# Performance work log

Measured on AMD Instinct MI355X. Metric: run time of the kernel, lower is better.

## Reference

```python
import jax, jax.numpy as jnp
import numpy as np

B, OP, MA, F_IN, F_OUT = 8, 400, 200, 64, 64


def setup_inputs() -> dict:
    key = jax.random.key(0)
    ks = jax.random.split(key, 8)
    x = jax.random.normal(ks[0], (B, OP, F_IN), dtype=jnp.float32)
    y = jax.random.normal(ks[1], (B, MA, F_IN), dtype=jnp.float32)
    z = jax.random.normal(ks[2], (B, OP, MA, F_IN), dtype=jnp.float32)
    op_ma_adj = jax.random.randint(ks[3], (B, OP, MA), 0, 2, dtype=jnp.int32)
    # xavier-uniform-ish params
    lim = float(np.sqrt(6.0 / (F_IN + F_OUT)))
    W_op = jax.random.uniform(ks[4], (F_IN, F_OUT), minval=-lim, maxval=lim, dtype=jnp.float32)
    W_ma = jax.random.uniform(ks[5], (F_IN, F_OUT), minval=-lim, maxval=lim, dtype=jnp.float32)
    W_edge = jax.random.uniform(ks[6], (F_IN, F_OUT), minval=-lim, maxval=lim, dtype=jnp.float32)
    lim_a = float(np.sqrt(6.0 / (1 + 3 * F_OUT)))
    att_vec = jax.random.uniform(ks[7], (3 * F_OUT,), minval=-lim_a, maxval=lim_a, dtype=jnp.float32)
    return {"x": x, "y": y, "z": z, "op_ma_adj": op_ma_adj,
            "W_op": W_op, "W_ma": W_ma, "W_edge": W_edge, "att_vec": att_vec}


def reference(x, y, z, op_ma_adj, W_op, W_ma, W_edge, att_vec):
    F = W_op.shape[1]
    h_op = jnp.einsum('bni,io->bno', x, W_op)                      # [B, op, F]
    h = jnp.einsum('bmi,io->bmo', y, W_ma)                         # [B, ma, F]
    h_edge = jnp.einsum('bnmi,io->bnmo', z, W_edge).transpose(0, 2, 1, 3)  # [B, ma, op, F]
    # attention score: concat([h_op, h_ma, h_edge]) @ a  ==  per-part dot products (no BxMAxOPx3F materialization)
    a_op, a_ma, a_edge = att_vec[:F], att_vec[F:2 * F], att_vec[2 * F:]
    e = (jnp.einsum('bnf,f->bn', h_op, a_op)[:, None, :]
         + jnp.einsum('bmf,f->bm', h, a_ma)[:, :, None]
         + jnp.einsum('bmnf,f->bmn', h_edge, a_edge))              # [B, ma, op]
    e = jax.nn.leaky_relu(e, negative_slope=0.01)
    adjT = op_ma_adj.transpose(0, 2, 1)                            # [B, ma, op]
    row_empty = jnp.all(adjT == 0, axis=-1, keepdims=True)         # [B, ma, 1]
    att = jnp.where(adjT > 0, e, -jnp.inf)
    att = jnp.where(row_empty, 0.0, att)                           # empty rows -> uniform softmax (matches torch)
    att = jax.nn.softmax(att, axis=-1)                             # [B, ma, op]
    h_op_edge = h_op[:, None, :, :] + h_edge                       # [B, ma, op, F]
    h_prime = jnp.einsum('bmn,bmnf->bmf', att, h_op_edge)          # [B, ma, F]
    h_prime = jnp.where(row_empty, 0.0, h_prime) + h
    return jax.nn.elu(h_prime)
```

## Files before the change

### kernel.cpp

```cpp
#include <hip/hip_runtime.h>
#include <math.h>

#define B_   8
#define OP_  400
#define MA_  200
#define ZROW (MA_ * 64)
#define NEGM -1.0e30f

__global__ __launch_bounds__(256) void precompute_k(
    const float* __restrict__ x, const float* __restrict__ y,
    const float* __restrict__ Wop, const float* __restrict__ Wma,
    const float* __restrict__ Wedge, const float* __restrict__ att,
    float* __restrict__ ws_we, float* __restrict__ ws_eop, float* __restrict__ ws_ema)
{
    __shared__ float w_s[192];
    const int tid = threadIdx.x, wv = tid >> 6, ln = tid & 63;
    if (tid < 192) {
        const int which = tid >> 6, i = tid & 63;
        const float* W = (which == 0) ? Wop : ((which == 1) ? Wma : Wedge);
        const float* a = att + which * 64;
        float acc = 0.f;
        #pragma unroll 8
        for (int f = 0; f < 64; ++f) acc = fmaf(W[i * 64 + f], a[f], acc);
        w_s[tid] = acc;
    }
    __syncthreads();
    if (blockIdx.x == 0 && tid < 64) ws_we[tid] = w_s[128 + tid];

    const int row = blockIdx.x * 4 + wv;
    if (row < B_ * OP_) {
        float s = x[(size_t)row * 64 + ln] * w_s[ln];
        #pragma unroll
        for (int o = 32; o > 0; o >>= 1) s += __shfl_xor(s, o, 64);
        if (ln == 0) ws_eop[row] = s;
    } else if (row < B_ * OP_ + B_ * MA_) {
        const int r2 = row - B_ * OP_;
        float s = y[(size_t)r2 * 64 + ln] * w_s[64 + ln];
        #pragma unroll
        for (int o = 32; o > 0; o >>= 1) s += __shfl_xor(s, o, 64);
        if (ln == 0) ws_ema[r2] = s;
    }
}

__global__ __launch_bounds__(256) void gat_fused(
    const float* __restrict__ x, const float* __restrict__ y,
    const float* __restrict__ z, const int* __restrict__ adj,
    const float* __restrict__ Wop, const float* __restrict__ Wma,
    const float* __restrict__ Wedge,
    const float* __restrict__ ws_we, const float* __restrict__ ws_eop,
    const float* __restrict__ ws_ema, float* __restrict__ out)
{
    __shared__ int   ln_s[4][104];
    __shared__ float le_s[4][104];
    __shared__ float mred[4], lred[4];
    __shared__ float vws[4][64], uws[4][64];
    __shared__ float vs_s[64], us_s[64], ys_s[64];
    __shared__ float pvt[4][64];

    const int tid = threadIdx.x, wv = tid >> 6, ln = tid & 63;
    const int bm = blockIdx.x;
    const int b = bm / MA_, m = bm % MA_;

    const float ema = ws_ema[bm];
    const float wl  = ws_we[ln];

    const int rbase = wv * 100;
    int cnt = 0;
    #pragma unroll
    for (int round = 0; round < 2; ++round) {
        const int lr = round * 64 + ln;
        const int n  = rbase + lr;
        bool a = false;
        if (lr < 100) a = (adj[((size_t)(b * OP_ + n)) * MA_ + m] != 0);
        const unsigned long long mask = __ballot(a);
        if (a) {
            const int pos = cnt + __popcll(mask & ((1ull << ln) - 1ull));
            ln_s[wv][pos] = n;
            le_s[wv][pos] = ws_eop[b * OP_ + n] + ema;
        }
        cnt += __popcll(mask);
    }
    const int cnt_p = (cnt + 3) & ~3;
    if (ln < cnt_p - cnt) {
        ln_s[wv][cnt + ln] = rbase;
        le_s[wv][cnt + ln] = NEGM;
    }

    const float* zb = z + ((size_t)b * OP_ * MA_ + m) * 64;
    const float* xb = x + (size_t)b * OP_ * 64;

    float M = NEGM, L = 0.f, v = 0.f, u = 0.f;

    #define UPD(zv, xv, eo) do {                                   \
        float s_ = (zv) * wl;                                      \
        s_ += __shfl_xor(s_, 1, 64);  s_ += __shfl_xor(s_, 2, 64); \
        s_ += __shfl_xor(s_, 4, 64);  s_ += __shfl_xor(s_, 8, 64); \
        s_ += __shfl_xor(s_, 16, 64); s_ += __shfl_xor(s_, 32, 64);\
        float e_ = s_ + (eo);                                      \
        e_ = (e_ >= 0.f) ? e_ : 0.01f * e_;                        \
        const float m2_ = fmaxf(M, e_);                            \
        const float c_  = __expf(M - m2_);                         \
        const float p_  = __expf(e_ - m2_);                        \
        L = fmaf(L, c_, p_);                                       \
        v = fmaf(v, c_, p_ * (zv));                                \
        u = fmaf(u, c_, p_ * (xv));                                \
        M = m2_;                                                   \
    } while (0)

    for (int i = 0; i < cnt_p; i += 4) {
        const int n0 = __builtin_amdgcn_readfirstlane(ln_s[wv][i + 0]);
        const int n1 = __builtin_amdgcn_readfirstlane(ln_s[wv][i + 1]);
        const int n2 = __builtin_amdgcn_readfirstlane(ln_s[wv][i + 2]);
        const int n3 = __builtin_amdgcn_readfirstlane(ln_s[wv][i + 3]);
        const float z0 = zb[(size_t)n0 * ZROW + ln];
        const float z1 = zb[(size_t)n1 * ZROW + ln];
        const float z2 = zb[(size_t)n2 * ZROW + ln];
        const float z3 = zb[(size_t)n3 * ZROW + ln];
        const float x0 = xb[(size_t)n0 * 64 + ln];
        const float x1 = xb[(size_t)n1 * 64 + ln];
        const float x2 = xb[(size_t)n2 * 64 + ln];
        const float x3 = xb[(size_t)n3 * 64 + ln];
        const float e0 = le_s[wv][i + 0];
        const float e1 = le_s[wv][i + 1];
        const float e2 = le_s[wv][i + 2];
        const float e3 = le_s[wv][i + 3];
        UPD(z0, x0, e0);
        UPD(z1, x1, e1);
        UPD(z2, x2, e2);
        UPD(z3, x3, e3);
    }
    #undef UPD

    if (ln == 0) { mred[wv] = M; lred[wv] = L; }
    vws[wv][ln] = v;
    uws[wv][ln] = u;
    __syncthreads();

    if (tid < 64) {
        const float Mg = fmaxf(fmaxf(mred[0], mred[1]), fmaxf(mred[2], mred[3]));
        const float c0 = __expf(mred[0] - Mg);
        const float c1 = __expf(mred[1] - Mg);
        const float c2 = __expf(mred[2] - Mg);
        const float c3 = __expf(mred[3] - Mg);
        const float Lg = c0 * lred[0] + c1 * lred[1] + c2 * lred[2] + c3 * lred[3];
        const float inv = (Lg > 0.f) ? (1.f / Lg) : 0.f;
        vs_s[tid] = (c0 * vws[0][tid] + c1 * vws[1][tid] +
                     c2 * vws[2][tid] + c3 * vws[3][tid]) * inv;
        us_s[tid] = (c0 * uws[0][tid] + c1 * uws[1][tid] +
                     c2 * uws[2][tid] + c3 * uws[3][tid]) * inv;
        ys_s[tid] = y[(size_t)bm * 64 + tid];
    }
    __syncthreads();

    {
        float acc = 0.f;
        const int i0 = wv * 16;
        #pragma unroll
        for (int k = 0; k < 16; ++k) {
            const int i = i0 + k;
            acc += vs_s[i] * Wedge[i * 64 + ln]
                 + us_s[i] * Wop[i * 64 + ln]
                 + ys_s[i] * Wma[i * 64 + ln];
        }
        pvt[wv][ln] = acc;
    }
    __syncthreads();
    if (tid < 64) {
        const float h = pvt[0][tid] + pvt[1][tid] + pvt[2][tid] + pvt[3][tid];
        out[(size_t)bm * 64 + tid] = (h > 0.f) ? h : (__expf(h) - 1.f);
    }
}

extern "C" void kernel_launch(void* const* d_in, const int* in_sizes, int n_in,
                              void* d_out, int out_size, void* d_ws, size_t ws_size,
                              hipStream_t stream) {
    const float* x     = (const float*)d_in[0];
    const float* y     = (const float*)d_in[1];
    const float* z     = (const float*)d_in[2];
    const int*   adj   = (const int*)d_in[3];
    const float* Wop   = (const float*)d_in[4];
    const float* Wma   = (const float*)d_in[5];
    const float* Wedge = (const float*)d_in[6];
    const float* att   = (const float*)d_in[7];

    float* ws     = (float*)d_ws;
    float* ws_we  = ws;
    float* ws_eop = ws + 64;
    float* ws_ema = ws + 64 + B_ * OP_;

    precompute_k<<<1200, 256, 0, stream>>>(
        x, y, Wop, Wma, Wedge, att, ws_we, ws_eop, ws_ema);
    gat_fused<<<B_ * MA_, 256, 0, stream>>>(
        x, y, z, adj, Wop, Wma, Wedge, ws_we, ws_eop, ws_ema, (float*)d_out);
}
```

Baseline: 250.2 us.

## Process four op rows per wave with float4 lanes and nontemporal z loads

Each wavefront now splits into four 16-lane groups, and each group handles a different neighbor row using 128-bit vector loads of z and x. Every group keeps its own online-softmax state, and the groups are merged with cross-lane shuffles at the end. The z loads are marked nontemporal, and the loop unrolls to 8 rows per iteration with padding up to a multiple of 8. The goal is fewer shuffle reductions per row and wider memory transactions on the z stream that dominates the cost, at the price of extra padding work and merge shuffles.

```diff
diff --git a/kernel.cpp b/kernel.cpp
--- a/kernel.cpp
+++ b/kernel.cpp
@@ -6,6 +6,8 @@
 #define MA_  200
 #define ZROW (MA_ * 64)
 #define NEGM -1.0e30f
+
+typedef float v4f __attribute__((ext_vector_type(4)));
 
 __global__ __launch_bounds__(256) void precompute_k(
     const float* __restrict__ x, const float* __restrict__ y,
@@ -50,19 +52,19 @@
     const float* __restrict__ ws_we, const float* __restrict__ ws_eop,
     const float* __restrict__ ws_ema, float* __restrict__ out)
 {
-    __shared__ int   ln_s[4][104];
-    __shared__ float le_s[4][104];
+    __shared__ int   ln_s[4][112];
+    __shared__ float le_s[4][112];
     __shared__ float mred[4], lred[4];
     __shared__ float vws[4][64], uws[4][64];
     __shared__ float vs_s[64], us_s[64], ys_s[64];
     __shared__ float pvt[4][64];
 
     const int tid = threadIdx.x, wv = tid >> 6, ln = tid & 63;
+    const int g = ln >> 4, q = ln & 15;
     const int bm = blockIdx.x;
     const int b = bm / MA_, m = bm % MA_;
 
     const float ema = ws_ema[bm];
-    const float wl  = ws_we[ln];
 
     const int rbase = wv * 100;
     int cnt = 0;
@@ -80,60 +82,74 @@
         }
         cnt += __popcll(mask);
     }
-    const int cnt_p = (cnt + 3) & ~3;
+    const int cnt_p = (cnt + 7) & ~7;
     if (ln < cnt_p - cnt) {
         ln_s[wv][cnt + ln] = rbase;
         le_s[wv][cnt + ln] = NEGM;
     }
 
-    const float* zb = z + ((size_t)b * OP_ * MA_ + m) * 64;
-    const float* xb = x + (size_t)b * OP_ * 64;
-
-    float M = NEGM, L = 0.f, v = 0.f, u = 0.f;
-
-    #define UPD(zv, xv, eo) do {                                   \
-        float s_ = (zv) * wl;                                      \
-        s_ += __shfl_xor(s_, 1, 64);  s_ += __shfl_xor(s_, 2, 64); \
-        s_ += __shfl_xor(s_, 4, 64);  s_ += __shfl_xor(s_, 8, 64); \
-        s_ += __shfl_xor(s_, 16, 64); s_ += __shfl_xor(s_, 32, 64);\
-        float e_ = s_ + (eo);                                      \
-        e_ = (e_ >= 0.f) ? e_ : 0.01f * e_;                        \
-        const float m2_ = fmaxf(M, e_);                            \
-        const float c_  = __expf(M - m2_);                         \
-        const float p_  = __expf(e_ - m2_);                        \
-        L = fmaf(L, c_, p_);                                       \
-        v = fmaf(v, c_, p_ * (zv));                                \
-        u = fmaf(u, c_, p_ * (xv));                                \
-        M = m2_;                                                   \
+    const float* zP = z + ((size_t)b * OP_ * MA_ + m) * 64;
+    const float* xP = x + (size_t)b * OP_ * 64;
+    const v4f wq = ((const v4f*)ws_we)[q];
+
+    v4f v = {0.f, 0.f, 0.f, 0.f}, u = {0.f, 0.f, 0.f, 0.f};
+    float M = NEGM, L = 0.f;
+
+    #define UPD(z4, x4, eo) do {                                               \
+        float s_ = fmaf((z4).x, wq.x, fmaf((z4).y, wq.y,                       \
+                   fmaf((z4).z, wq.z, (z4).w * wq.w)));                        \
+        s_ += __shfl_xor(s_, 1, 64); s_ += __shfl_xor(s_, 2, 64);              \
+        s_ += __shfl_xor(s_, 4, 64); s_ += __shfl_xor(s_, 8, 64);              \
+        float e_ = s_ + (eo);                                                  \
+        e_ = (e_ >= 0.f) ? e_ : 0.01f * e_;                                    \
+        const float m2_ = fmaxf(M, e_);                                        \
+        const float c_  = __expf(M - m2_);                                     \
+        const float p_  = __expf(e_ - m2_);                                    \
+        L = fmaf(L, c_, p_);                                                   \
+        v = v * c_ + (z4) * p_;                                                \
+        u = u * c_ + (x4) * p_;                                                \
+        M = m2_;                                                               \
     } while (0)
 
-    for (int i = 0; i < cnt_p; i += 4) {
-        const int n0 = __builtin_amdgcn_readfirstlane(ln_s[wv][i + 0]);
-        const int n1 = __builtin_amdgcn_readfirstlane(ln_s[wv][i + 1]);
-        const int n2 = __builtin_amdgcn_readfirstlane(ln_s[wv][i + 2]);
-        const int n3 = __builtin_amdgcn_readfirstlane(ln_s[wv][i + 3]);
-        const float z0 = zb[(size_t)n0 * ZROW + ln];
-        const float z1 = zb[(size_t)n1 * ZROW + ln];
-        const float z2 = zb[(size_t)n2 * ZROW + ln];
-        const float z3 = zb[(size_t)n3 * ZROW + ln];
-        const float x0 = xb[(size_t)n0 * 64 + ln];
-        const float x1 = xb[(size_t)n1 * 64 + ln];
-        const float x2 = xb[(size_t)n2 * 64 + ln];
-        const float x3 = xb[(size_t)n3 * 64 + ln];
-        const float e0 = le_s[wv][i + 0];
-        const float e1 = le_s[wv][i + 1];
-        const float e2 = le_s[wv][i + 2];
-        const float e3 = le_s[wv][i + 3];
-        UPD(z0, x0, e0);
-        UPD(z1, x1, e1);
-        UPD(z2, x2, e2);
-        UPD(z3, x3, e3);
+    for (int i = 0; i < cnt_p; i += 8) {
+        const int na = ln_s[wv][i + g];
+        const int nb = ln_s[wv][i + 4 + g];
+        const float ea = le_s[wv][i + g];
+        const float eb = le_s[wv][i + 4 + g];
+        const v4f za = __builtin_nontemporal_load(
+            (const v4f*)(zP + (size_t)na * ZROW) + q);
+        const v4f zb4 = __builtin_nontemporal_load(
+            (const v4f*)(zP + (size_t)nb * ZROW) + q);
+        const v4f xa  = *((const v4f*)(xP + ((size_t)na << 6)) + q);
+        const v4f xb4 = *((const v4f*)(xP + ((size_t)nb << 6)) + q);
+        UPD(za, xa, ea);
+        UPD(zb4, xb4, eb);
     }
     #undef UPD
 
-    if (ln == 0) { mred[wv] = M; lred[wv] = L; }
-    vws[wv][ln] = v;
-    uws[wv][ln] = u;
+    float Mw = M;
+    Mw = fmaxf(Mw, __shfl_xor(Mw, 16, 64));
+    Mw = fmaxf(Mw, __shfl_xor(Mw, 32, 64));
+    const float cg = __expf(M - Mw);
+    float Lw = L * cg;
+    Lw += __shfl_xor(Lw, 16, 64);
+    Lw += __shfl_xor(Lw, 32, 64);
+    v *= cg;
+    u *= cg;
+    v.x += __shfl_xor(v.x, 16, 64); v.y += __shfl_xor(v.y, 16, 64);
+    v.z += __shfl_xor(v.z, 16, 64); v.w += __shfl_xor(v.w, 16, 64);
+    v.x += __shfl_xor(v.x, 32, 64); v.y += __shfl_xor(v.y, 32, 64);
+    v.z += __shfl_xor(v.z, 32, 64); v.w += __shfl_xor(v.w, 32, 64);
+    u.x += __shfl_xor(u.x, 16, 64); u.y += __shfl_xor(u.y, 16, 64);
+    u.z += __shfl_xor(u.z, 16, 64); u.w += __shfl_xor(u.w, 16, 64);
+    u.x += __shfl_xor(u.x, 32, 64); u.y += __shfl_xor(u.y, 32, 64);
+    u.z += __shfl_xor(u.z, 32, 64); u.w += __shfl_xor(u.w, 32, 64);
+
+    if (ln < 16) {
+        ((v4f*)vws[wv])[q] = v;
+        ((v4f*)uws[wv])[q] = u;
+    }
+    if (ln == 0) { mred[wv] = Mw; lred[wv] = Lw; }
     __syncthreads();
 
     if (tid < 64) {
```

New measurement: 240.1 us. 1.04x faster.
